# Kernel tuning notes

Hardware: AMD Instinct MI355X
Metric: run time of the kernel (lower is better)

Reference implementation:

```python
import jax, jax.numpy as jnp
import numpy as np

B, S, D = 32, 4096, 64
EPS_DIV = 1e-8
EPS_LN = 1e-5  # torch LayerNorm default


def setup_inputs() -> dict:
    key = jax.random.key(0)
    k1, k2, k3 = jax.random.split(key, 3)
    C = jax.random.normal(k1, (B, S, D), dtype=jnp.float32)
    V = jax.random.normal(k2, (B, S, D), dtype=jnp.float32)
    W = jax.random.normal(k3, (B, S, D), dtype=jnp.float32)
    time_mod = jnp.ones((1, 1, D), dtype=jnp.float32) * 0.5  # matches init: ones * 0.5
    ln_gamma = jnp.ones((D,), dtype=jnp.float32)
    ln_beta = jnp.zeros((D,), dtype=jnp.float32)
    return {"C": C, "V": V, "W": W, "time_mod": time_mod,
            "ln_gamma": ln_gamma, "ln_beta": ln_beta}


def reference(C, V, W, time_mod, ln_gamma, ln_beta):
    # Precompute elementwise quantities once (fused, no per-step kernels)
    decay = jax.nn.sigmoid(W * time_mod)        # [B,S,D]
    eC = jnp.exp(C)                             # [B,S,D]

    # scan over sequence axis; move S to the front for lax.scan
    xs = (jnp.swapaxes(decay, 0, 1),            # [S,B,D]
          jnp.swapaxes(eC, 0, 1),
          jnp.swapaxes(V, 0, 1))

    a0 = jnp.zeros((C.shape[0], 1), dtype=C.dtype)
    b0 = jnp.zeros((C.shape[0], C.shape[2]), dtype=C.dtype)

    def step(carry, x):
        a, b = carry
        d, ec, v = x                            # each [B,D]
        a = jnp.mean(d, axis=1, keepdims=True) * a + jnp.sum(ec, axis=1, keepdims=True)
        b = d * b + ec * v
        return (a, b), b / (a + EPS_DIV)

    _, ys = jax.lax.scan(step, (a0, b0), xs)    # ys: [S,B,D]
    result = jnp.swapaxes(ys, 0, 1)             # [B,S,D]

    # LayerNorm over last dim
    mu = jnp.mean(result, axis=-1, keepdims=True)
    var = jnp.var(result, axis=-1, keepdims=True)
    normed = (result - mu) * jax.lax.rsqrt(var + EPS_LN)
    return normed * ln_gamma + ln_beta
```

## Files before the change

### kernel.cpp

```cpp
#include <hip/hip_runtime.h>

constexpr int B = 32, S = 4096, D = 64;
constexpr float EPS_DIV = 1e-8f;
constexpr float EPS_LN  = 1e-5f;

constexpr int NCG = 512;
constexpr int LG  = S / NCG;
constexpr int CPL = NCG / 64;

__device__ __forceinline__ float sigmoid_f(float x) {
    return __builtin_amdgcn_rcpf(1.f + __expf(-x));
}

__device__ __forceinline__ void gsum2(float& x, float& y) {
#pragma unroll
    for (int m = 1; m < 16; m <<= 1) {
        x += __shfl_xor(x, m, 64);
        y += __shfl_xor(y, m, 64);
    }
}

__global__ __launch_bounds__(256) void k1g(
    const float4* __restrict__ C4, const float4* __restrict__ V4,
    const float4* __restrict__ W4, const float* __restrict__ TM,
    float2* __restrict__ MQstep,
    float*  __restrict__ Mc, float* __restrict__ Qc,
    float4* __restrict__ Pt4, float4* __restrict__ Ot4)
{
    __shared__ float sp[64][17];
    __shared__ float so[64][17];

    const int t = threadIdx.x;
    const int g = t >> 4;
    const int r = t & 15;
    const int G = blockIdx.x * 16 + g;
    const int b = G >> 9;
    const int c = G & (NCG - 1);
    const int c0 = (blockIdx.x & 31) * 16;
    const int s0 = c * LG;
    const size_t base = (size_t)(b * S + s0) * 16 + r;
    const float4 tm = reinterpret_cast<const float4*>(TM)[r];

    float M = 1.f, Q = 0.f;
    float4 P = {1.f, 1.f, 1.f, 1.f}, O = {0.f, 0.f, 0.f, 0.f};
#pragma unroll
    for (int i = 0; i < LG; ++i) {
        const size_t idx = base + (size_t)i * 16;
        const float4 w = W4[idx], cc = C4[idx], v = V4[idx];
        float4 dg, ec;
        dg.x = sigmoid_f(w.x * tm.x); dg.y = sigmoid_f(w.y * tm.y);
        dg.z = sigmoid_f(w.z * tm.z); dg.w = sigmoid_f(w.w * tm.w);
        ec.x = __expf(cc.x); ec.y = __expf(cc.y);
        ec.z = __expf(cc.z); ec.w = __expf(cc.w);
        float sd = (dg.x + dg.y) + (dg.z + dg.w);
        float se = (ec.x + ec.y) + (ec.z + ec.w);
        gsum2(sd, se);
        const float mm = sd * (1.f / 64.f);
        if (r == 0) MQstep[b * S + s0 + i] = make_float2(mm, se);
        M *= mm;
        Q  = fmaf(mm, Q, se);
        P.x *= dg.x; P.y *= dg.y; P.z *= dg.z; P.w *= dg.w;
        O.x = fmaf(dg.x, O.x, ec.x * v.x);
        O.y = fmaf(dg.y, O.y, ec.y * v.y);
        O.z = fmaf(dg.z, O.z, ec.z * v.z);
        O.w = fmaf(dg.w, O.w, ec.w * v.w);
    }
    if (r == 0) { Mc[G] = M; Qc[G] = Q; }

    sp[4*r+0][g] = P.x; sp[4*r+1][g] = P.y; sp[4*r+2][g] = P.z; sp[4*r+3][g] = P.w;
    so[4*r+0][g] = O.x; so[4*r+1][g] = O.y; so[4*r+2][g] = O.z; so[4*r+3][g] = O.w;
    __syncthreads();
    const int d  = t >> 2;
    const int cq = t & 3;
    const float4 vp = make_float4(sp[d][cq*4+0], sp[d][cq*4+1],
                                  sp[d][cq*4+2], sp[d][cq*4+3]);
    const float4 vo = make_float4(so[d][cq*4+0], so[d][cq*4+1],
                                  so[d][cq*4+2], so[d][cq*4+3]);
    const size_t row4 = (size_t)(b * D + d) * (NCG / 4);
    Pt4[row4 + (c0 >> 2) + cq] = vp;
    Ot4[row4 + (c0 >> 2) + cq] = vo;
}

__global__ __launch_bounds__(256) void k2(
    const float*  __restrict__ Mc,  const float*  __restrict__ Qc,
    const float4* __restrict__ Pt4, const float4* __restrict__ Ot4,
    float4* __restrict__ aIn4,
    float4* __restrict__ bIn4)
{
    const int wq   = threadIdx.x >> 6;
    const int lane = threadIdx.x & 63;

    if (blockIdx.x < 512) {
        const int W = blockIdx.x * 4 + wq;
        const int b = W >> 6, d = W & 63;
        const size_t row4 = (size_t)(b * D + d) * (NCG / 4);
        const float4 pA = Pt4[row4 + lane*2],     pB = Pt4[row4 + lane*2 + 1];
        const float4 oA = Ot4[row4 + lane*2],     oB = Ot4[row4 + lane*2 + 1];
        float pj[CPL] = {pA.x, pA.y, pA.z, pA.w, pB.x, pB.y, pB.z, pB.w};
        float oj[CPL] = {oA.x, oA.y, oA.z, oA.w, oB.x, oB.y, oB.z, oB.w};
        float p = 1.f, o = 0.f;
#pragma unroll
        for (int j = 0; j < CPL; ++j) { o = fmaf(pj[j], o, oj[j]); p = pj[j] * p; }
#pragma unroll
        for (int s = 1; s < 64; s <<= 1) {
            const float pp = __shfl_up(p, s, 64);
            const float oo = __shfl_up(o, s, 64);
            if (lane >= s) { o = fmaf(p, oo, o); p = p * pp; }
        }
        float oe = __shfl_up(o, 1, 64);
        if (lane == 0) oe = 0.f;
        float bv = oe, ob[CPL];
#pragma unroll
        for (int j = 0; j < CPL; ++j) { ob[j] = bv; bv = fmaf(pj[j], bv, oj[j]); }
        bIn4[row4 + lane*2]     = make_float4(ob[0], ob[1], ob[2], ob[3]);
        bIn4[row4 + lane*2 + 1] = make_float4(ob[4], ob[5], ob[6], ob[7]);
    } else {
        const int v = (blockIdx.x - 512) * 4 + wq;
        if (v >= B) return;
        const int b = v;
        const float4* Mc4 = reinterpret_cast<const float4*>(Mc) + b * (NCG / 4);
        const float4* Qc4 = reinterpret_cast<const float4*>(Qc) + b * (NCG / 4);
        const float4 mA = Mc4[lane*2], mB = Mc4[lane*2 + 1];
        const float4 qA = Qc4[lane*2], qB = Qc4[lane*2 + 1];
        float mj[CPL] = {mA.x, mA.y, mA.z, mA.w, mB.x, mB.y, mB.z, mB.w};
        float qj[CPL] = {qA.x, qA.y, qA.z, qA.w, qB.x, qB.y, qB.z, qB.w};
        float m = 1.f, q = 0.f;
#pragma unroll
        for (int j = 0; j < CPL; ++j) { q = fmaf(mj[j], q, qj[j]); m = mj[j] * m; }
#pragma unroll
        for (int s = 1; s < 64; s <<= 1) {
            const float mm = __shfl_up(m, s, 64);
            const float qq = __shfl_up(q, s, 64);
            if (lane >= s) { q = fmaf(m, qq, q); m = m * mm; }
        }
        float qe = __shfl_up(q, 1, 64);
        if (lane == 0) qe = 0.f;
        float a = qe, ab[CPL];
#pragma unroll
        for (int j = 0; j < CPL; ++j) { ab[j] = a; a = fmaf(mj[j], a, qj[j]); }
        aIn4[b * (NCG / 4) + lane*2]     = make_float4(ab[0], ab[1], ab[2], ab[3]);
        aIn4[b * (NCG / 4) + lane*2 + 1] = make_float4(ab[4], ab[5], ab[6], ab[7]);
    }
}

__global__ __launch_bounds__(256) void k3g(
    const float4* __restrict__ C4, const float4* __restrict__ V4,
    const float4* __restrict__ W4, const float* __restrict__ TM,
    const float* __restrict__ Gam, const float* __restrict__ Bet,
    const float2* __restrict__ MQstep,
    const float* __restrict__ aIn, const float4* __restrict__ bInT4,
    float4* __restrict__ out4)
{
    __shared__ float sb[64][16];

    const int t = threadIdx.x;
    const int b  = blockIdx.x >> 5;
    const int c0 = (blockIdx.x & 31) * 16;
    {
        const int d = t >> 2, cq = t & 3;
        const float4 ld = bInT4[(size_t)(b * D + d) * (NCG / 4) + (c0 >> 2) + cq];
        *reinterpret_cast<float4*>(&sb[d][cq * 4]) = ld;
    }
    __syncthreads();

    const int g = t >> 4;
    const int r = t & 15;
    const int c = c0 + g;
    const int s0 = c * LG;
    const size_t base = (size_t)(b * S + s0) * 16 + r;
    const float4 tm = reinterpret_cast<const float4*>(TM)[r];
    const float4 g4 = reinterpret_cast<const float4*>(Gam)[r];
    const float4 b4 = reinterpret_cast<const float4*>(Bet)[r];

    float a = aIn[b * NCG + c];
    float4 bv = make_float4(sb[4*r+0][g], sb[4*r+1][g],
                            sb[4*r+2][g], sb[4*r+3][g]);
#pragma unroll
    for (int i = 0; i < LG; ++i) {
        const size_t idx = base + (size_t)i * 16;
        const float4 w = W4[idx], cc = C4[idx], v = V4[idx];
        float4 dg, ec;
        dg.x = sigmoid_f(w.x * tm.x); dg.y = sigmoid_f(w.y * tm.y);
        dg.z = sigmoid_f(w.z * tm.z); dg.w = sigmoid_f(w.w * tm.w);
        ec.x = __expf(cc.x); ec.y = __expf(cc.y);
        ec.z = __expf(cc.z); ec.w = __expf(cc.w);
        const float2 mq = MQstep[b * S + s0 + i];
        a = fmaf(mq.x, a, mq.y);
        bv.x = fmaf(dg.x, bv.x, ec.x * v.x);
        bv.y = fmaf(dg.y, bv.y, ec.y * v.y);
        bv.z = fmaf(dg.z, bv.z, ec.z * v.z);
        bv.w = fmaf(dg.w, bv.w, ec.w * v.w);
        const float inva = __builtin_amdgcn_rcpf(a + EPS_DIV);
        float4 y;
        y.x = bv.x * inva; y.y = bv.y * inva;
        y.z = bv.z * inva; y.w = bv.w * inva;
        float sy = (y.x + y.y) + (y.z + y.w);
        float sq = fmaf(y.x, y.x, y.y * y.y) + fmaf(y.z, y.z, y.w * y.w);
        gsum2(sy, sq);
        const float mu  = sy * (1.f / 64.f);
        const float var = fmaf(-mu, mu, sq * (1.f / 64.f));
        const float rs  = __builtin_amdgcn_rsqf(fmaxf(var, 0.f) + EPS_LN);
        float4 o;
        o.x = fmaf((y.x - mu) * rs, g4.x, b4.x);
        o.y = fmaf((y.y - mu) * rs, g4.y, b4.y);
        o.z = fmaf((y.z - mu) * rs, g4.z, b4.z);
        o.w = fmaf((y.w - mu) * rs, g4.w, b4.w);
        out4[idx] = o;
    }
}

__global__ __launch_bounds__(64) void k_naive(
    const float* __restrict__ Cp, const float* __restrict__ Vp,
    const float* __restrict__ Wp, const float* __restrict__ TM,
    const float* __restrict__ Gam, const float* __restrict__ Bet,
    float* __restrict__ out)
{
    const int b = blockIdx.x;
    const int lane = threadIdx.x;
    const float tm = TM[lane], g = Gam[lane], bt = Bet[lane];
    float a = 0.f, bv = 0.f;
    for (int s = 0; s < S; ++s) {
        const size_t idx = ((size_t)b * S + s) * D + lane;
        const float wv = Wp[idx], cv = Cp[idx], vv = Vp[idx];
        const float dg = sigmoid_f(wv * tm);
        const float ec = __expf(cv);
        float sd = dg, se = ec;
#pragma unroll
        for (int m = 1; m < 64; m <<= 1) {
            sd += __shfl_xor(sd, m, 64);
            se += __shfl_xor(se, m, 64);
        }
        a  = fmaf(sd * (1.f / 64.f), a, se);
        bv = fmaf(dg, bv, ec * vv);
        const float y = bv * __builtin_amdgcn_rcpf(a + EPS_DIV);
        float sy = y, sq = y * y;
#pragma unroll
        for (int m = 1; m < 64; m <<= 1) {
            sy += __shfl_xor(sy, m, 64);
            sq += __shfl_xor(sq, m, 64);
        }
        const float mu  = sy * (1.f / 64.f);
        const float var = fmaf(-mu, mu, sq * (1.f / 64.f));
        const float rs  = __builtin_amdgcn_rsqf(fmaxf(var, 0.f) + EPS_LN);
        out[idx] = fmaf((y - mu) * rs, g, bt);
    }
}

extern "C" void kernel_launch(void* const* d_in, const int* in_sizes, int n_in,
                              void* d_out, int out_size, void* d_ws, size_t ws_size,
                              hipStream_t stream) {
    const float* Cp  = (const float*)d_in[0];
    const float* Vp  = (const float*)d_in[1];
    const float* Wp  = (const float*)d_in[2];
    const float* TM  = (const float*)d_in[3];
    const float* Gam = (const float*)d_in[4];
    const float* Bet = (const float*)d_in[5];
    float* out = (float*)d_out;
    float* wsf = (float*)d_ws;

    const size_t f_mq   = (size_t)B * S * 2;
    const size_t f_scG  = (size_t)B * NCG;
    const size_t f_vecG = (size_t)B * NCG * D;
    const size_t needG  = (f_mq + 3 * f_scG + 3 * f_vecG) * sizeof(float);

    if (ws_size >= needG) {
        float2* MQstep = (float2*)wsf;
        float* Mc  = wsf + f_mq;
        float* Qc  = Mc + f_scG;
        float* Pt  = Qc + f_scG;
        float* Ot  = Pt + f_vecG;
        float* aIn = Ot + f_vecG;
        float* bIn = aIn + f_scG;

        const int groups = B * NCG;
        const dim3 blk(256);
        const dim3 grd(groups / 16);

        k1g<<<grd, blk, 0, stream>>>((const float4*)Cp, (const float4*)Vp,
                                     (const float4*)Wp, TM, MQstep, Mc, Qc,
                                     (float4*)Pt, (float4*)Ot);
        k2<<<dim3(512 + 16), blk, 0, stream>>>(Mc, Qc, (const float4*)Pt,
                                               (const float4*)Ot,
                                               (float4*)aIn, (float4*)bIn);
        k3g<<<grd, blk, 0, stream>>>((const float4*)Cp, (const float4*)Vp,
                                     (const float4*)Wp, TM, Gam, Bet, MQstep,
                                     aIn, (const float4*)bIn, (float4*)out);
        return;
    }

    k_naive<<<dim3(B), dim3(64), 0, stream>>>(Cp, Vp, Wp, TM, Gam, Bet, out);
}
```

Before: 46.58 us.

## Fuse three scan phases into one cooperative kernel with grid syncs

```diff
diff --git a/kernel.cpp b/kernel.cpp
--- a/kernel.cpp
+++ b/kernel.cpp
@@ -1,4 +1,7 @@
 #include <hip/hip_runtime.h>
+#include <hip/hip_cooperative_groups.h>
+
+namespace cg = cooperative_groups;
 
 constexpr int B = 32, S = 4096, D = 64;
 constexpr float EPS_DIV = 1e-8f;
@@ -20,12 +23,16 @@
     }
 }
 
-__global__ __launch_bounds__(256) void k1g(
+__global__ __launch_bounds__(256, 4) void k_fused(
     const float4* __restrict__ C4, const float4* __restrict__ V4,
     const float4* __restrict__ W4, const float* __restrict__ TM,
+    const float* __restrict__ Gam, const float* __restrict__ Bet,
     float2* __restrict__ MQstep,
     float*  __restrict__ Mc, float* __restrict__ Qc,
-    float4* __restrict__ Pt4, float4* __restrict__ Ot4)
+    float4* __restrict__ Pt4, float4* __restrict__ Ot4,
+    float*  __restrict__ aIn,
+    float4* __restrict__ bInT4,
+    float4* __restrict__ out4)
 {
     __shared__ float sp[64][17];
     __shared__ float so[64][17];
@@ -41,6 +48,7 @@
     const size_t base = (size_t)(b * S + s0) * 16 + r;
     const float4 tm = reinterpret_cast<const float4*>(TM)[r];
 
+    float4 dgr[LG], evr[LG];
     float M = 1.f, Q = 0.f;
     float4 P = {1.f, 1.f, 1.f, 1.f}, O = {0.f, 0.f, 0.f, 0.f};
 #pragma unroll
@@ -60,13 +68,174 @@
         M *= mm;
         Q  = fmaf(mm, Q, se);
         P.x *= dg.x; P.y *= dg.y; P.z *= dg.z; P.w *= dg.w;
+        float4 ev;
+        ev.x = ec.x * v.x; ev.y = ec.y * v.y;
+        ev.z = ec.z * v.z; ev.w = ec.w * v.w;
+        O.x = fmaf(dg.x, O.x, ev.x);
+        O.y = fmaf(dg.y, O.y, ev.y);
+        O.z = fmaf(dg.z, O.z, ev.z);
+        O.w = fmaf(dg.w, O.w, ev.w);
+        dgr[i] = dg; evr[i] = ev;
+    }
+    if (r == 0) { Mc[G] = M; Qc[G] = Q; }
+
+    sp[4*r+0][g] = P.x; sp[4*r+1][g] = P.y; sp[4*r+2][g] = P.z; sp[4*r+3][g] = P.w;
+    so[4*r+0][g] = O.x; so[4*r+1][g] = O.y; so[4*r+2][g] = O.z; so[4*r+3][g] = O.w;
+    __syncthreads();
+    {
+        const int d  = t >> 2;
+        const int cq = t & 3;
+        const float4 vp = make_float4(sp[d][cq*4+0], sp[d][cq*4+1],
+                                      sp[d][cq*4+2], sp[d][cq*4+3]);
+        const float4 vo = make_float4(so[d][cq*4+0], so[d][cq*4+1],
+                                      so[d][cq*4+2], so[d][cq*4+3]);
+        const size_t row4 = (size_t)(b * D + d) * (NCG / 4);
+        Pt4[row4 + (c0 >> 2) + cq] = vp;
+        Ot4[row4 + (c0 >> 2) + cq] = vo;
+    }
+
+    cg::this_grid().sync();
+
+    {
+        const int wid  = blockIdx.x * 4 + (t >> 6);
+        const int lane = t & 63;
+        if (wid < 2048) {
+            const int vb = wid >> 6, vd = wid & 63;
+            const size_t row4 = (size_t)(vb * D + vd) * (NCG / 4);
+            const float4 pA = Pt4[row4 + lane*2], pB = Pt4[row4 + lane*2 + 1];
+            const float4 oA = Ot4[row4 + lane*2], oB = Ot4[row4 + lane*2 + 1];
+            float pj[CPL] = {pA.x, pA.y, pA.z, pA.w, pB.x, pB.y, pB.z, pB.w};
+            float oj[CPL] = {oA.x, oA.y, oA.z, oA.w, oB.x, oB.y, oB.z, oB.w};
+            float p = 1.f, o = 0.f;
+#pragma unroll
+            for (int j = 0; j < CPL; ++j) { o = fmaf(pj[j], o, oj[j]); p = pj[j] * p; }
+#pragma unroll
+            for (int s = 1; s < 64; s <<= 1) {
+                const float pp = __shfl_up(p, s, 64);
+                const float oo = __shfl_up(o, s, 64);
+                if (lane >= s) { o = fmaf(p, oo, o); p = p * pp; }
+            }
+            float oe = __shfl_up(o, 1, 64);
+            if (lane == 0) oe = 0.f;
+            float bv = oe, ob[CPL];
+#pragma unroll
+            for (int j = 0; j < CPL; ++j) { ob[j] = bv; bv = fmaf(pj[j], bv, oj[j]); }
+            bInT4[row4 + lane*2]     = make_float4(ob[0], ob[1], ob[2], ob[3]);
+            bInT4[row4 + lane*2 + 1] = make_float4(ob[4], ob[5], ob[6], ob[7]);
+        } else if (wid < 2048 + B) {
+            const int sb_ = wid - 2048;
+            const float4* Mc4 = reinterpret_cast<const float4*>(Mc) + sb_ * (NCG / 4);
+            const float4* Qc4 = reinterpret_cast<const float4*>(Qc) + sb_ * (NCG / 4);
+            const float4 mA = Mc4[lane*2], mB = Mc4[lane*2 + 1];
+            const float4 qA = Qc4[lane*2], qB = Qc4[lane*2 + 1];
+            float mj[CPL] = {mA.x, mA.y, mA.z, mA.w, mB.x, mB.y, mB.z, mB.w};
+            float qj[CPL] = {qA.x, qA.y, qA.z, qA.w, qB.x, qB.y, qB.z, qB.w};
+            float m = 1.f, q = 0.f;
+#pragma unroll
+            for (int j = 0; j < CPL; ++j) { q = fmaf(mj[j], q, qj[j]); m = mj[j] * m; }
+#pragma unroll
+            for (int s = 1; s < 64; s <<= 1) {
+                const float mm2 = __shfl_up(m, s, 64);
+                const float qq2 = __shfl_up(q, s, 64);
+                if (lane >= s) { q = fmaf(m, qq2, q); m = m * mm2; }
+            }
+            float qe = __shfl_up(q, 1, 64);
+            if (lane == 0) qe = 0.f;
+            float a = qe, ab[CPL];
+#pragma unroll
+            for (int j = 0; j < CPL; ++j) { ab[j] = a; a = fmaf(mj[j], a, qj[j]); }
+            float4* aIn4 = reinterpret_cast<float4*>(aIn) + sb_ * (NCG / 4);
+            aIn4[lane*2]     = make_float4(ab[0], ab[1], ab[2], ab[3]);
+            aIn4[lane*2 + 1] = make_float4(ab[4], ab[5], ab[6], ab[7]);
+        }
+    }
+
+    cg::this_grid().sync();
+
+    {
+        const int d = t >> 2, cq = t & 3;
+        const float4 ld = bInT4[(size_t)(b * D + d) * (NCG / 4) + (c0 >> 2) + cq];
+        sp[d][cq*4+0] = ld.x; sp[d][cq*4+1] = ld.y;
+        sp[d][cq*4+2] = ld.z; sp[d][cq*4+3] = ld.w;
+    }
+    __syncthreads();
+
+    const float4 g4 = reinterpret_cast<const float4*>(Gam)[r];
+    const float4 b4 = reinterpret_cast<const float4*>(Bet)[r];
+    float a = aIn[b * NCG + c];
+    float4 bv = make_float4(sp[4*r+0][g], sp[4*r+1][g],
+                            sp[4*r+2][g], sp[4*r+3][g]);
+#pragma unroll
+    for (int i = 0; i < LG; ++i) {
+        const float2 mq = MQstep[b * S + s0 + i];
+        a = fmaf(mq.x, a, mq.y);
+        const float4 dg = dgr[i], ev = evr[i];
+        bv.x = fmaf(dg.x, bv.x, ev.x);
+        bv.y = fmaf(dg.y, bv.y, ev.y);
+        bv.z = fmaf(dg.z, bv.z, ev.z);
+        bv.w = fmaf(dg.w, bv.w, ev.w);
+        const float inva = __builtin_amdgcn_rcpf(a + EPS_DIV);
+        float4 y;
+        y.x = bv.x * inva; y.y = bv.y * inva;
+        y.z = bv.z * inva; y.w = bv.w * inva;
+        float sy = (y.x + y.y) + (y.z + y.w);
+        float sq = fmaf(y.x, y.x, y.y * y.y) + fmaf(y.z, y.z, y.w * y.w);
+        gsum2(sy, sq);
+        const float mu  = sy * (1.f / 64.f);
+        const float var = fmaf(-mu, mu, sq * (1.f / 64.f));
+        const float rs  = __builtin_amdgcn_rsqf(fmaxf(var, 0.f) + EPS_LN);
+        float4 o;
+        o.x = fmaf((y.x - mu) * rs, g4.x, b4.x);
+        o.y = fmaf((y.y - mu) * rs, g4.y, b4.y);
+        o.z = fmaf((y.z - mu) * rs, g4.z, b4.z);
+        o.w = fmaf((y.w - mu) * rs, g4.w, b4.w);
+        out4[base + (size_t)i * 16] = o;
+    }
+}
+
+__global__ __launch_bounds__(256) void k1g(
+    const float4* __restrict__ C4, const float4* __restrict__ V4,
+    const float4* __restrict__ W4, const float* __restrict__ TM,
+    float2* __restrict__ MQstep,
+    float*  __restrict__ Mc, float* __restrict__ Qc,
+    float4* __restrict__ Pt4, float4* __restrict__ Ot4)
+{
+    __shared__ float sp[64][17];
+    __shared__ float so[64][17];
+    const int t = threadIdx.x;
+    const int g = t >> 4;
+    const int r = t & 15;
+    const int G = blockIdx.x * 16 + g;
+    const int b = G >> 9;
+    const int c = G & (NCG - 1);
+    const int c0 = (blockIdx.x & 31) * 16;
+    const int s0 = c * LG;
+    const size_t base = (size_t)(b * S + s0) * 16 + r;
+    const float4 tm = reinterpret_cast<const float4*>(TM)[r];
+    float M = 1.f, Q = 0.f;
+    float4 P = {1.f, 1.f, 1.f, 1.f}, O = {0.f, 0.f, 0.f, 0.f};
+#pragma unroll
+    for (int i = 0; i < LG; ++i) {
+        const size_t idx = base + (size_t)i * 16;
+        const float4 w = W4[idx], cc = C4[idx], v = V4[idx];
+        float4 dg, ec;
+        dg.x = sigmoid_f(w.x * tm.x); dg.y = sigmoid_f(w.y * tm.y);
+        dg.z = sigmoid_f(w.z * tm.z); dg.w = sigmoid_f(w.w * tm.w);
+        ec.x = __expf(cc.x); ec.y = __expf(cc.y);
+        ec.z = __expf(cc.z); ec.w = __expf(cc.w);
+        float sd = (dg.x + dg.y) + (dg.z + dg.w);
+        float se = (ec.x + ec.y) + (ec.z + ec.w);
+        gsum2(sd, se);
+        const float mm = sd * (1.f / 64.f);
+        if (r == 0) MQstep[b * S + s0 + i] = make_float2(mm, se);
+        M *= mm; Q = fmaf(mm, Q, se);
+        P.x *= dg.x; P.y *= dg.y; P.z *= dg.z; P.w *= dg.w;
         O.x = fmaf(dg.x, O.x, ec.x * v.x);
         O.y = fmaf(dg.y, O.y, ec.y * v.y);
         O.z = fmaf(dg.z, O.z, ec.z * v.z);
         O.w = fmaf(dg.w, O.w, ec.w * v.w);
     }
     if (r == 0) { Mc[G] = M; Qc[G] = Q; }
-
     sp[4*r+0][g] = P.x; sp[4*r+1][g] = P.y; sp[4*r+2][g] = P.z; sp[4*r+3][g] = P.w;
     so[4*r+0][g] = O.x; so[4*r+1][g] = O.y; so[4*r+2][g] = O.z; so[4*r+3][g] = O.w;
     __syncthreads();
@@ -84,18 +253,16 @@
 __global__ __launch_bounds__(256) void k2(
     const float*  __restrict__ Mc,  const float*  __restrict__ Qc,
     const float4* __restrict__ Pt4, const float4* __restrict__ Ot4,
-    float4* __restrict__ aIn4,
-    float4* __restrict__ bIn4)
+    float4* __restrict__ aIn4, float4* __restrict__ bIn4)
 {
     const int wq   = threadIdx.x >> 6;
     const int lane = threadIdx.x & 63;
-
     if (blockIdx.x < 512) {
         const int W = blockIdx.x * 4 + wq;
         const int b = W >> 6, d = W & 63;
         const size_t row4 = (size_t)(b * D + d) * (NCG / 4);
-        const float4 pA = Pt4[row4 + lane*2],     pB = Pt4[row4 + lane*2 + 1];
-        const float4 oA = Ot4[row4 + lane*2],     oB = Ot4[row4 + lane*2 + 1];
+        const float4 pA = Pt4[row4 + lane*2], pB = Pt4[row4 + lane*2 + 1];
+        const float4 oA = Ot4[row4 + lane*2], oB = Ot4[row4 + lane*2 + 1];
         float pj[CPL] = {pA.x, pA.y, pA.z, pA.w, pB.x, pB.y, pB.z, pB.w};
         float oj[CPL] = {oA.x, oA.y, oA.z, oA.w, oB.x, oB.y, oB.z, oB.w};
         float p = 1.f, o = 0.f;
@@ -117,9 +284,8 @@
     } else {
         const int v = (blockIdx.x - 512) * 4 + wq;
         if (v >= B) return;
-        const int b = v;
-        const float4* Mc4 = reinterpret_cast<const float4*>(Mc) + b * (NCG / 4);
-        const float4* Qc4 = reinterpret_cast<const float4*>(Qc) + b * (NCG / 4);
+        const float4* Mc4 = reinterpret_cast<const float4*>(Mc) + v * (NCG / 4);
+        const float4* Qc4 = reinterpret_cast<const float4*>(Qc) + v * (NCG / 4);
         const float4 mA = Mc4[lane*2], mB = Mc4[lane*2 + 1];
         const float4 qA = Qc4[lane*2], qB = Qc4[lane*2 + 1];
         float mj[CPL] = {mA.x, mA.y, mA.z, mA.w, mB.x, mB.y, mB.z, mB.w};
@@ -138,8 +304,8 @@
         float a = qe, ab[CPL];
 #pragma unroll
         for (int j = 0; j < CPL; ++j) { ab[j] = a; a = fmaf(mj[j], a, qj[j]); }
-        aIn4[b * (NCG / 4) + lane*2]     = make_float4(ab[0], ab[1], ab[2], ab[3]);
-        aIn4[b * (NCG / 4) + lane*2 + 1] = make_float4(ab[4], ab[5], ab[6], ab[7]);
+        aIn4[v * (NCG / 4) + lane*2]     = make_float4(ab[0], ab[1], ab[2], ab[3]);
+        aIn4[v * (NCG / 4) + lane*2 + 1] = make_float4(ab[4], ab[5], ab[6], ab[7]);
     }
 }
 
@@ -152,7 +318,6 @@
     float4* __restrict__ out4)
 {
     __shared__ float sb[64][16];
-
     const int t = threadIdx.x;
     const int b  = blockIdx.x >> 5;
     const int c0 = (blockIdx.x & 31) * 16;
@@ -162,7 +327,6 @@
         *reinterpret_cast<float4*>(&sb[d][cq * 4]) = ld;
     }
     __syncthreads();
-
     const int g = t >> 4;
     const int r = t & 15;
     const int c = c0 + g;
@@ -171,7 +335,6 @@
     const float4 tm = reinterpret_cast<const float4*>(TM)[r];
     const float4 g4 = reinterpret_cast<const float4*>(Gam)[r];
     const float4 b4 = reinterpret_cast<const float4*>(Bet)[r];
-
     float a = aIn[b * NCG + c];
     float4 bv = make_float4(sb[4*r+0][g], sb[4*r+1][g],
                             sb[4*r+2][g], sb[4*r+3][g]);
@@ -272,9 +435,34 @@
         float* aIn = Ot + f_vecG;
         float* bIn = aIn + f_scG;
 
-        const int groups = B * NCG;
         const dim3 blk(256);
-        const dim3 grd(groups / 16);
+        const dim3 grd(B * NCG / 16);
+
+        int maxPerCU = 0, nCU = 0;
+        hipError_t e1 = hipOccupancyMaxActiveBlocksPerMultiprocessor(
+            &maxPerCU, k_fused, 256, 0);
+        hipError_t e2 = hipDeviceGetAttribute(
+            &nCU, hipDeviceAttributeMultiprocessorCount, 0);
+        if (e1 == hipSuccess && e2 == hipSuccess &&
+            (size_t)maxPerCU * (size_t)nCU >= (size_t)grd.x) {
+            const float4* C4 = (const float4*)Cp;
+            const float4* V4 = (const float4*)Vp;
+            const float4* W4 = (const float4*)Wp;
+            float4* Pt4 = (float4*)Pt;
+            float4* Ot4 = (float4*)Ot;
+            float4* bIn4 = (float4*)bIn;
+            float4* out4 = (float4*)out;
+            void* args[] = {
+                (void*)&C4, (void*)&V4, (void*)&W4,
+                (void*)&TM, (void*)&Gam, (void*)&Bet,
+                (void*)&MQstep, (void*)&Mc, (void*)&Qc,
+                (void*)&Pt4, (void*)&Ot4, (void*)&aIn,
+                (void*)&bIn4, (void*)&out4
+            };
+            hipError_t le = hipLaunchCooperativeKernel(
+                (const void*)k_fused, grd, blk, args, 0, stream);
+            if (le == hipSuccess) return;
+        }
 
         k1g<<<grd, blk, 0, stream>>>((const float4*)Cp, (const float4*)Vp,
                                      (const float4*)Wp, TM, MQstep, Mc, Qc,
```

New measurement: 46.91 us. Within noise of the previous version (+0.7%).

## Cache decay and ec*v as fp16 pairs for pass 3, double chunk count

Applied to the files above, without the earlier changes.

```diff
diff --git a/kernel.cpp b/kernel.cpp
--- a/kernel.cpp
+++ b/kernel.cpp
@@ -1,12 +1,16 @@
 #include <hip/hip_runtime.h>
+#include <hip/hip_fp16.h>
 
 constexpr int B = 32, S = 4096, D = 64;
 constexpr float EPS_DIV = 1e-8f;
 constexpr float EPS_LN  = 1e-5f;
 
-constexpr int NCG = 512;
+constexpr int NCG = 1024;
 constexpr int LG  = S / NCG;
 constexpr int CPL = NCG / 64;
+constexpr int BPB = NCG / 16;
+
+struct alignas(16) H2x4 { __half2 a, b, c, d; };
 
 __device__ __forceinline__ float sigmoid_f(float x) {
     return __builtin_amdgcn_rcpf(1.f + __expf(-x));
@@ -20,12 +24,13 @@
     }
 }
 
-__global__ __launch_bounds__(256) void k1g(
+__global__ __launch_bounds__(256) void k1h(
     const float4* __restrict__ C4, const float4* __restrict__ V4,
     const float4* __restrict__ W4, const float* __restrict__ TM,
     float2* __restrict__ MQstep,
     float*  __restrict__ Mc, float* __restrict__ Qc,
-    float4* __restrict__ Pt4, float4* __restrict__ Ot4)
+    float4* __restrict__ Pt4, float4* __restrict__ Ot4,
+    H2x4*   __restrict__ dgev)
 {
     __shared__ float sp[64][17];
     __shared__ float so[64][17];
@@ -34,9 +39,9 @@
     const int g = t >> 4;
     const int r = t & 15;
     const int G = blockIdx.x * 16 + g;
-    const int b = G >> 9;
+    const int b = G >> 10;
     const int c = G & (NCG - 1);
-    const int c0 = (blockIdx.x & 31) * 16;
+    const int c0 = (blockIdx.x & (BPB - 1)) * 16;
     const int s0 = c * LG;
     const size_t base = (size_t)(b * S + s0) * 16 + r;
     const float4 tm = reinterpret_cast<const float4*>(TM)[r];
@@ -59,11 +64,21 @@
         if (r == 0) MQstep[b * S + s0 + i] = make_float2(mm, se);
         M *= mm;
         Q  = fmaf(mm, Q, se);
-        P.x *= dg.x; P.y *= dg.y; P.z *= dg.z; P.w *= dg.w;
-        O.x = fmaf(dg.x, O.x, ec.x * v.x);
-        O.y = fmaf(dg.y, O.y, ec.y * v.y);
-        O.z = fmaf(dg.z, O.z, ec.z * v.z);
-        O.w = fmaf(dg.w, O.w, ec.w * v.w);
+        H2x4 hq;
+        hq.a = __floats2half2_rn(dg.x, ec.x * v.x);
+        hq.b = __floats2half2_rn(dg.y, ec.y * v.y);
+        hq.c = __floats2half2_rn(dg.z, ec.z * v.z);
+        hq.d = __floats2half2_rn(dg.w, ec.w * v.w);
+        dgev[idx] = hq;
+        const float2 f0 = __half22float2(hq.a);
+        const float2 f1 = __half22float2(hq.b);
+        const float2 f2 = __half22float2(hq.c);
+        const float2 f3 = __half22float2(hq.d);
+        P.x *= f0.x; P.y *= f1.x; P.z *= f2.x; P.w *= f3.x;
+        O.x = fmaf(f0.x, O.x, f0.y);
+        O.y = fmaf(f1.x, O.y, f1.y);
+        O.z = fmaf(f2.x, O.z, f2.y);
+        O.w = fmaf(f3.x, O.w, f3.y);
     }
     if (r == 0) { Mc[G] = M; Qc[G] = Q; }
 
@@ -94,10 +109,14 @@
         const int W = blockIdx.x * 4 + wq;
         const int b = W >> 6, d = W & 63;
         const size_t row4 = (size_t)(b * D + d) * (NCG / 4);
-        const float4 pA = Pt4[row4 + lane*2],     pB = Pt4[row4 + lane*2 + 1];
-        const float4 oA = Ot4[row4 + lane*2],     oB = Ot4[row4 + lane*2 + 1];
-        float pj[CPL] = {pA.x, pA.y, pA.z, pA.w, pB.x, pB.y, pB.z, pB.w};
-        float oj[CPL] = {oA.x, oA.y, oA.z, oA.w, oB.x, oB.y, oB.z, oB.w};
+        float pj[CPL], oj[CPL];
+#pragma unroll
+        for (int q4 = 0; q4 < 4; ++q4) {
+            const float4 pv = Pt4[row4 + lane*4 + q4];
+            const float4 ov = Ot4[row4 + lane*4 + q4];
+            pj[q4*4+0] = pv.x; pj[q4*4+1] = pv.y; pj[q4*4+2] = pv.z; pj[q4*4+3] = pv.w;
+            oj[q4*4+0] = ov.x; oj[q4*4+1] = ov.y; oj[q4*4+2] = ov.z; oj[q4*4+3] = ov.w;
+        }
         float p = 1.f, o = 0.f;
 #pragma unroll
         for (int j = 0; j < CPL; ++j) { o = fmaf(pj[j], o, oj[j]); p = pj[j] * p; }
@@ -109,21 +128,29 @@
         }
         float oe = __shfl_up(o, 1, 64);
         if (lane == 0) oe = 0.f;
-        float bv = oe, ob[CPL];
-#pragma unroll
-        for (int j = 0; j < CPL; ++j) { ob[j] = bv; bv = fmaf(pj[j], bv, oj[j]); }
-        bIn4[row4 + lane*2]     = make_float4(ob[0], ob[1], ob[2], ob[3]);
-        bIn4[row4 + lane*2 + 1] = make_float4(ob[4], ob[5], ob[6], ob[7]);
+        float bv = oe;
+#pragma unroll
+        for (int q4 = 0; q4 < 4; ++q4) {
+            float4 w;
+            w.x = bv; bv = fmaf(pj[q4*4+0], bv, oj[q4*4+0]);
+            w.y = bv; bv = fmaf(pj[q4*4+1], bv, oj[q4*4+1]);
+            w.z = bv; bv = fmaf(pj[q4*4+2], bv, oj[q4*4+2]);
+            w.w = bv; bv = fmaf(pj[q4*4+3], bv, oj[q4*4+3]);
+            bIn4[row4 + lane*4 + q4] = w;
+        }
     } else {
         const int v = (blockIdx.x - 512) * 4 + wq;
         if (v >= B) return;
-        const int b = v;
-        const float4* Mc4 = reinterpret_cast<const float4*>(Mc) + b * (NCG / 4);
-        const float4* Qc4 = reinterpret_cast<const float4*>(Qc) + b * (NCG / 4);
-        const float4 mA = Mc4[lane*2], mB = Mc4[lane*2 + 1];
-        const float4 qA = Qc4[lane*2], qB = Qc4[lane*2 + 1];
-        float mj[CPL] = {mA.x, mA.y, mA.z, mA.w, mB.x, mB.y, mB.z, mB.w};
-        float qj[CPL] = {qA.x, qA.y, qA.z, qA.w, qB.x, qB.y, qB.z, qB.w};
+        const float4* Mc4 = reinterpret_cast<const float4*>(Mc) + v * (NCG / 4);
+        const float4* Qc4 = reinterpret_cast<const float4*>(Qc) + v * (NCG / 4);
+        float mj[CPL], qj[CPL];
+#pragma unroll
+        for (int q4 = 0; q4 < 4; ++q4) {
+            const float4 mv = Mc4[lane*4 + q4];
+            const float4 qv = Qc4[lane*4 + q4];
+            mj[q4*4+0] = mv.x; mj[q4*4+1] = mv.y; mj[q4*4+2] = mv.z; mj[q4*4+3] = mv.w;
+            qj[q4*4+0] = qv.x; qj[q4*4+1] = qv.y; qj[q4*4+2] = qv.z; qj[q4*4+3] = qv.w;
+        }
         float m = 1.f, q = 0.f;
 #pragma unroll
         for (int j = 0; j < CPL; ++j) { q = fmaf(mj[j], q, qj[j]); m = mj[j] * m; }
@@ -135,31 +162,37 @@
         }
         float qe = __shfl_up(q, 1, 64);
         if (lane == 0) qe = 0.f;
-        float a = qe, ab[CPL];
-#pragma unroll
-        for (int j = 0; j < CPL; ++j) { ab[j] = a; a = fmaf(mj[j], a, qj[j]); }
-        aIn4[b * (NCG / 4) + lane*2]     = make_float4(ab[0], ab[1], ab[2], ab[3]);
-        aIn4[b * (NCG / 4) + lane*2 + 1] = make_float4(ab[4], ab[5], ab[6], ab[7]);
-    }
-}
-
-__global__ __launch_bounds__(256) void k3g(
-    const float4* __restrict__ C4, const float4* __restrict__ V4,
-    const float4* __restrict__ W4, const float* __restrict__ TM,
+        float a = qe;
+        float4* out4 = reinterpret_cast<float4*>(aIn4) + v * (NCG / 4);
+#pragma unroll
+        for (int q4 = 0; q4 < 4; ++q4) {
+            float4 w;
+            w.x = a; a = fmaf(mj[q4*4+0], a, qj[q4*4+0]);
+            w.y = a; a = fmaf(mj[q4*4+1], a, qj[q4*4+1]);
+            w.z = a; a = fmaf(mj[q4*4+2], a, qj[q4*4+2]);
+            w.w = a; a = fmaf(mj[q4*4+3], a, qj[q4*4+3]);
+            out4[lane*4 + q4] = w;
+        }
+    }
+}
+
+__global__ __launch_bounds__(256) void k3h(
+    const H2x4* __restrict__ dgev,
     const float* __restrict__ Gam, const float* __restrict__ Bet,
     const float2* __restrict__ MQstep,
     const float* __restrict__ aIn, const float4* __restrict__ bInT4,
     float4* __restrict__ out4)
 {
-    __shared__ float sb[64][16];
+    __shared__ float sb[64][17];
 
     const int t = threadIdx.x;
-    const int b  = blockIdx.x >> 5;
-    const int c0 = (blockIdx.x & 31) * 16;
+    const int b  = blockIdx.x >> 6;
+    const int c0 = (blockIdx.x & (BPB - 1)) * 16;
     {
         const int d = t >> 2, cq = t & 3;
         const float4 ld = bInT4[(size_t)(b * D + d) * (NCG / 4) + (c0 >> 2) + cq];
-        *reinterpret_cast<float4*>(&sb[d][cq * 4]) = ld;
+        sb[d][cq*4+0] = ld.x; sb[d][cq*4+1] = ld.y;
+        sb[d][cq*4+2] = ld.z; sb[d][cq*4+3] = ld.w;
     }
     __syncthreads();
 
@@ -168,7 +201,6 @@
     const int c = c0 + g;
     const int s0 = c * LG;
     const size_t base = (size_t)(b * S + s0) * 16 + r;
-    const float4 tm = reinterpret_cast<const float4*>(TM)[r];
     const float4 g4 = reinterpret_cast<const float4*>(Gam)[r];
     const float4 b4 = reinterpret_cast<const float4*>(Bet)[r];
 
@@ -178,18 +210,17 @@
 #pragma unroll
     for (int i = 0; i < LG; ++i) {
         const size_t idx = base + (size_t)i * 16;
-        const float4 w = W4[idx], cc = C4[idx], v = V4[idx];
-        float4 dg, ec;
-        dg.x = sigmoid_f(w.x * tm.x); dg.y = sigmoid_f(w.y * tm.y);
-        dg.z = sigmoid_f(w.z * tm.z); dg.w = sigmoid_f(w.w * tm.w);
-        ec.x = __expf(cc.x); ec.y = __expf(cc.y);
-        ec.z = __expf(cc.z); ec.w = __expf(cc.w);
+        const H2x4 hq = dgev[idx];
+        const float2 f0 = __half22float2(hq.a);
+        const float2 f1 = __half22float2(hq.b);
+        const float2 f2 = __half22float2(hq.c);
+        const float2 f3 = __half22float2(hq.d);
         const float2 mq = MQstep[b * S + s0 + i];
         a = fmaf(mq.x, a, mq.y);
-        bv.x = fmaf(dg.x, bv.x, ec.x * v.x);
-        bv.y = fmaf(dg.y, bv.y, ec.y * v.y);
-        bv.z = fmaf(dg.z, bv.z, ec.z * v.z);
-        bv.w = fmaf(dg.w, bv.w, ec.w * v.w);
+        bv.x = fmaf(f0.x, bv.x, f0.y);
+        bv.y = fmaf(f1.x, bv.y, f1.y);
+        bv.z = fmaf(f2.x, bv.z, f2.y);
+        bv.w = fmaf(f3.x, bv.w, f3.y);
         const float inva = __builtin_amdgcn_rcpf(a + EPS_DIV);
         float4 y;
         y.x = bv.x * inva; y.y = bv.y * inva;
@@ -261,9 +292,11 @@
     const size_t f_mq   = (size_t)B * S * 2;
     const size_t f_scG  = (size_t)B * NCG;
     const size_t f_vecG = (size_t)B * NCG * D;
-    const size_t needG  = (f_mq + 3 * f_scG + 3 * f_vecG) * sizeof(float);
-
-    if (ws_size >= needG) {
+    const size_t f_base = f_mq + 3 * f_scG + 3 * f_vecG;
+    const size_t f_dgev = (size_t)B * S * D;
+    const size_t needH  = (f_base + f_dgev) * sizeof(float);
+
+    if (ws_size >= needH) {
         float2* MQstep = (float2*)wsf;
         float* Mc  = wsf + f_mq;
         float* Qc  = Mc + f_scG;
@@ -271,19 +304,18 @@
         float* Ot  = Pt + f_vecG;
         float* aIn = Ot + f_vecG;
         float* bIn = aIn + f_scG;
-
-        const int groups = B * NCG;
+        H2x4* dgev = (H2x4*)(wsf + f_base);
+
         const dim3 blk(256);
-        const dim3 grd(groups / 16);
-
-        k1g<<<grd, blk, 0, stream>>>((const float4*)Cp, (const float4*)Vp,
+        const dim3 grd(B * NCG / 16);
+
+        k1h<<<grd, blk, 0, stream>>>((const float4*)Cp, (const float4*)Vp,
                                      (const float4*)Wp, TM, MQstep, Mc, Qc,
-                                     (float4*)Pt, (float4*)Ot);
-        k2<<<dim3(512 + 16), blk, 0, stream>>>(Mc, Qc, (const float4*)Pt,
-                                               (const float4*)Ot,
-                                               (float4*)aIn, (float4*)bIn);
-        k3g<<<grd, blk, 0, stream>>>((const float4*)Cp, (const float4*)Vp,
-                                     (const float4*)Wp, TM, Gam, Bet, MQstep,
+                                     (float4*)Pt, (float4*)Ot, dgev);
+        k2<<<dim3(512 + 8), blk, 0, stream>>>(Mc, Qc, (const float4*)Pt,
+                                              (const float4*)Ot,
+                                              (float4*)aIn, (float4*)bIn);
+        k3h<<<grd, blk, 0, stream>>>(dgev, Gam, Bet, MQstep,
                                      aIn, (const float4*)bIn, (float4*)out);
         return;
     }
```

Measured after the change: 49.01 us. 5.2% more time.
